# Performance work log

Measured on AMD Instinct MI355X. Metric: run time of the kernel, lower is better.

## Reference

```python
import jax, jax.numpy as jnp
import numpy as np

DIM = 1024
NUM_HEADS = 16
HEAD_DIM = DIM // NUM_HEADS
B, NQ, NKV = 8, 1024, 1024


def setup_inputs() -> dict:
    key = jax.random.key(0)
    ks = jax.random.split(key, 6)
    std = 1.0 / np.sqrt(DIM)
    return {
        "x": jax.random.normal(ks[0], (B, NQ, DIM), dtype=jnp.float32),
        "context": jax.random.normal(ks[1], (B, NKV, DIM), dtype=jnp.float32),
        "Wq": jax.random.normal(ks[2], (DIM, DIM), dtype=jnp.float32) * std,
        "bq": jnp.zeros((DIM,), dtype=jnp.float32),
        "Wk": jax.random.normal(ks[3], (DIM, DIM), dtype=jnp.float32) * std,
        "bk": jnp.zeros((DIM,), dtype=jnp.float32),
        "Wv": jax.random.normal(ks[4], (DIM, DIM), dtype=jnp.float32) * std,
        "bv": jnp.zeros((DIM,), dtype=jnp.float32),
        "Wo": jax.random.normal(ks[5], (DIM, DIM), dtype=jnp.float32) * std,
        "bo": jnp.zeros((DIM,), dtype=jnp.float32),
    }


def _split_heads(t):
    # [B, N, D] -> [B, H, N, Hd]
    b, n, _ = t.shape
    return t.reshape(b, n, NUM_HEADS, HEAD_DIM).transpose(0, 2, 1, 3)


def reference(x, context, Wq, bq, Wk, bk, Wv, bv, Wo, bo):
    scale = HEAD_DIM ** -0.5
    q = _split_heads(x @ Wq + bq)        # [B,H,Nq,Hd]
    k = _split_heads(context @ Wk + bk)  # [B,H,Nk,Hd]
    v = _split_heads(context @ Wv + bv)  # [B,H,Nk,Hd]
    # scaled dot-product attention
    scores = jnp.einsum("bhqd,bhkd->bhqk", q, k) * scale
    attn = jax.nn.softmax(scores, axis=-1)
    out = jnp.einsum("bhqk,bhkd->bhqd", attn, v)  # [B,H,Nq,Hd]
    out = out.transpose(0, 2, 1, 3).reshape(x.shape[0], x.shape[1], DIM)
    return out @ Wo + bo
```

## Files before the change

kernel.cpp:

```cpp
#include <hip/hip_runtime.h>
#include <stdint.h>

using bf16x8 = __attribute__((ext_vector_type(8))) short;
using f32x4  = __attribute__((ext_vector_type(4))) float;
using f32x2  = __attribute__((ext_vector_type(2))) float;
using u16    = unsigned short;
using u16x4  = __attribute__((ext_vector_type(4))) unsigned short;
using u16x8  = __attribute__((ext_vector_type(8))) unsigned short;
using bf16x2v = __attribute__((ext_vector_type(2))) __bf16;

#define LOG2E 1.4426950408889634f

static __device__ __forceinline__ u16 bf16r(float f) {
  union { __bf16 h; u16 u; } v; v.h = (__bf16)f; return v.u;
}
static __device__ __forceinline__ unsigned pk2(float a, float b) {
  union { bf16x2v h; unsigned u; } r;
  r.h = __builtin_convertvector((f32x2){a, b}, bf16x2v);
  return r.u;
}
static __device__ __forceinline__ u16x4 pk4(float a, float b, float c, float d) {
  union { unsigned u[2]; u16x4 v; } r;
  r.u[0] = pk2(a, b); r.u[1] = pk2(c, d);
  return r.v;
}

static __device__ __forceinline__ void async_ld16(u16* lds, const u16* g) {
  __builtin_amdgcn_global_load_lds(
      (const __attribute__((address_space(1))) void*)g,
      (__attribute__((address_space(3))) void*)lds,
      16, 0, 0);
}

static __device__ __forceinline__ f32x4 mfma16(bf16x8 a, bf16x8 b, f32x4 c) {
  return __builtin_amdgcn_mfma_f32_16x16x32_bf16(a, b, c, 0, 0, 0);
}

__global__ void prep_kernel(const float* __restrict__ x, const float* __restrict__ ctx,
                            const float* __restrict__ W0, const float* __restrict__ W1,
                            const float* __restrict__ W2, const float* __restrict__ W3,
                            u16* __restrict__ Xb, u16* __restrict__ Cb,
                            u16* __restrict__ T0, u16* __restrict__ T1,
                            u16* __restrict__ T2, u16* __restrict__ T3) {
  int bid = blockIdx.x;
  int t = threadIdx.x;
  if (bid < 4096) {
    const int n4 = 2097152;
    int i = bid * 256 + t;
    const int stride = 4096 * 256;
#pragma unroll
    for (int it = 0; it < 4; ++it, i += stride) {
      const float4* src = (i < n4) ? ((const float4*)x + i) : ((const float4*)ctx + (i - n4));
      u16x4* dst = (i < n4) ? ((u16x4*)Xb + i) : ((u16x4*)Cb + (i - n4));
      float4 v = *src;
      *dst = pk4(v.x, v.y, v.z, v.w);
    }
    return;
  }
  int b2 = bid - 4096;
  int z = b2 >> 8, rem = b2 & 255;
  const float* W = (z == 0) ? W0 : (z == 1) ? W1 : (z == 2) ? W2 : W3;
  u16* T = (z == 0) ? T0 : (z == 1) ? T1 : (z == 2) ? T2 : T3;
  __shared__ float tile[64][65];
  int k0 = (rem & 15) * 64, n0 = (rem >> 4) * 64;
#pragma unroll
  for (int i = 0; i < 4; ++i) {
    int kl = i * 16 + (t >> 4); int nl = (t & 15) * 4;
    float4 v = *(const float4*)(W + (size_t)(k0 + kl) * 1024 + n0 + nl);
    tile[kl][nl] = v.x; tile[kl][nl + 1] = v.y; tile[kl][nl + 2] = v.z; tile[kl][nl + 3] = v.w;
  }
  __syncthreads();
#pragma unroll
  for (int i = 0; i < 16; ++i) {
    int idx = i * 256 + t; int nl = idx >> 6; int kl = idx & 63;
    T[(size_t)(n0 + nl) * 1024 + k0 + kl] = bf16r(tile[kl][nl]);
  }
}

__global__ __launch_bounds__(256) void proj_gemm_kernel(
    const u16* __restrict__ Xb, const u16* __restrict__ Cb,
    const u16* __restrict__ Wqt, const u16* __restrict__ Wkt, const u16* __restrict__ Wvt,
    const float* __restrict__ bq, const float* __restrict__ bk, const float* __restrict__ bv,
    u16* __restrict__ Qo, u16* __restrict__ Ko, u16* __restrict__ Vo) {
  __shared__ u16 smem[16896];
  u16* sA = smem;
  u16* sB = smem + 8192;
  int z = blockIdx.z;
  const u16* A    = (z == 0) ? Xb : Cb;
  const u16* Bt   = (z == 0) ? Wqt : (z == 1) ? Wkt : Wvt;
  const float* bias = (z == 0) ? bq : (z == 1) ? bk : bv;
  int m0 = blockIdx.x * 128, n0 = blockIdx.y * 128;
  int t = threadIdx.x, w = t >> 6, lane = t & 63, quad = lane >> 4, lc = lane & 15;
  int wm = (w & 1) * 64, wn = (w >> 1) * 64;
  int sx = lc & 7;

  f32x4 acc[4][4];
  f32x4 z4 = {0.f, 0.f, 0.f, 0.f};
#pragma unroll
  for (int i = 0; i < 4; ++i)
#pragma unroll
    for (int j = 0; j < 4; ++j) acc[i][j] = z4;

  int srow = t >> 3;
  int swz  = (t & 7) ^ (srow & 7);
  const u16* Ag = A  + (size_t)(m0 + srow) * 1024 + swz * 8;
  const u16* Bg = Bt + (size_t)(n0 + srow) * 1024 + swz * 8;
  u16* la = sA + t * 8;
  u16* lb = sB + t * 8;

  for (int kt = 0; kt < 16; ++kt) {
    __syncthreads();
#pragma unroll
    for (int i = 0; i < 4; ++i) {
      async_ld16(la + i * 2048, Ag + (size_t)i * 32 * 1024);
      async_ld16(lb + i * 2048, Bg + (size_t)i * 32 * 1024);
    }
    Ag += 64; Bg += 64;
    asm volatile("s_waitcnt vmcnt(0)" ::: "memory");
    __syncthreads();
#pragma unroll
    for (int ks = 0; ks < 2; ++ks) {
      bf16x8 af[4], bfr[4];
#pragma unroll
      for (int i = 0; i < 4; ++i)
        af[i]  = *(const bf16x8*)(sA + (wm + i * 16 + lc) * 64 + (((ks * 4 + quad) ^ sx)) * 8);
#pragma unroll
      for (int i = 0; i < 4; ++i)
        bfr[i] = *(const bf16x8*)(sB + (wn + i * 16 + lc) * 64 + (((ks * 4 + quad) ^ sx)) * 8);
#pragma unroll
      for (int qi = 0; qi < 4; ++qi)
#pragma unroll
        for (int nj = 0; nj < 4; ++nj) acc[qi][nj] = mfma16(af[qi], bfr[nj], acc[qi][nj]);
    }
  }

  if (z < 2) {
    u16* dst = (z == 0) ? Qo : Ko;
    float scl = (z == 0) ? 0.125f * LOG2E : 1.0f;
#pragma unroll
    for (int qi = 0; qi < 4; ++qi)
#pragma unroll
      for (int nj = 0; nj < 4; ++nj) {
        int n = n0 + wn + nj * 16 + lc;
        float bvv = bias[n];
        int hh = n >> 6, d = n & 63;
#pragma unroll
        for (int r = 0; r < 4; ++r) {
          int m = m0 + wm + qi * 16 + quad * 4 + r;
          int bb = m >> 10, pos = m & 1023;
          float v = (acc[qi][nj][r] + bvv) * scl;
          dst[((size_t)(bb * 16 + hh) * 1024 + pos) * 64 + d] = bf16r(v);
        }
      }
  } else {
    __syncthreads();
    u16* Tw = smem + w * (64 * 66);
    int hh = (n0 + wn) >> 6;
    int mb = m0 + wm; int bb = mb >> 10; int pos0 = mb & 1023;
#pragma unroll
    for (int qi = 0; qi < 4; ++qi)
#pragma unroll
      for (int nj = 0; nj < 4; ++nj) {
        int lcc = nj * 16 + lc;
        float bvv = bias[n0 + wn + lcc];
#pragma unroll
        for (int r = 0; r < 4; ++r) {
          int lr = qi * 16 + quad * 4 + r;
          Tw[lr * 66 + lcc] = bf16r(acc[qi][nj][r] + bvv);
        }
      }
#pragma unroll
    for (int i = 0; i < 8; ++i) {
      int dl = i * 8 + (lane >> 3); int kv0 = (lane & 7) * 8;
      u16x8 pk;
#pragma unroll
      for (int j = 0; j < 8; ++j) pk[j] = Tw[(kv0 + j) * 66 + dl];
      *(u16x8*)(Vo + ((size_t)(bb * 16 + hh) * 64 + dl) * 1024 + pos0 + kv0) = pk;
    }
  }
}

__global__ __launch_bounds__(256, 3) void attn_kernel(const u16* __restrict__ Qb,
                                                      const u16* __restrict__ Kb,
                                                      const u16* __restrict__ Vt,
                                                      u16* __restrict__ Ab) {
  __shared__ u16 smem[24576];
  u16* sP = smem + 16384;
  int bid = blockIdx.x;
  int bh = (bid & 7) | ((bid >> 6) << 3);
  int qt = (bid >> 3) & 7;
  int bb = bh >> 4, hh = bh & 15;
  int t = threadIdx.x, w = t >> 6, lane = t & 63, quad = lane >> 4, lc = lane & 15;

  const u16* Qg = Qb + ((size_t)bh * 1024 + qt * 128 + w * 32) * 64;
  bf16x8 qf[2][2];
#pragma unroll
  for (int qi = 0; qi < 2; ++qi)
#pragma unroll
    for (int ks = 0; ks < 2; ++ks)
      qf[qi][ks] = *(const bf16x8*)(Qg + (qi * 16 + lc) * 64 + ks * 32 + quad * 8);

  f32x4 O[4][2];
  f32x4 z4 = {0.f, 0.f, 0.f, 0.f};
#pragma unroll
  for (int dj = 0; dj < 4; ++dj) { O[dj][0] = z4; O[dj][1] = z4; }
  float l_lane[2] = {0.f, 0.f};

  const u16* Kg = Kb + (size_t)bh * 65536;
  const u16* Vg = Vt + (size_t)bh * 65536;
  int r0 = t >> 3, gs = t & 7;

  auto STAGE = [&](int b, int kt) {
    u16* sKb = smem + b * 8192;
    u16* sVb = sKb + 4096;
#pragma unroll
    for (int i = 0; i < 2; ++i) {
      int r = r0 + i * 32;
      async_ld16(sKb + i * 2048 + t * 8, Kg + (size_t)(kt * 64 + r) * 64 + (gs ^ (r & 7)) * 8);
    }
#pragma unroll
    for (int i = 0; i < 2; ++i) {
      int d = r0 + i * 32;
      async_ld16(sVb + i * 2048 + t * 8, Vg + (size_t)d * 1024 + kt * 64 + (gs ^ (d & 7)) * 8);
    }
  };

  STAGE(0, 0);

  for (int kt = 0; kt < 16; ++kt) {
    int cur = kt & 1;
    __builtin_amdgcn_s_barrier();
    if (kt < 15) {
      STAGE(cur ^ 1, kt + 1);
      asm volatile("s_waitcnt vmcnt(8)" ::: "memory");
    } else {
      asm volatile("s_waitcnt vmcnt(0)" ::: "memory");
    }
    __builtin_amdgcn_s_barrier();

    const u16* sK = smem + cur * 8192;
    const u16* sV = sK + 4096;

    f32x4 s[4][2];
#pragma unroll
    for (int kj = 0; kj < 4; ++kj) { s[kj][0] = z4; s[kj][1] = z4; }
    __builtin_amdgcn_s_setprio(1);
#pragma unroll
    for (int kj = 0; kj < 4; ++kj) {
      int kv = kj * 16 + lc;
#pragma unroll
      for (int ks = 0; ks < 2; ++ks) {
        bf16x8 a = *(const bf16x8*)(sK + kv * 64 + ((ks * 4 + quad) ^ (kv & 7)) * 8);
        s[kj][0] = mfma16(a, qf[0][ks], s[kj][0]);
        s[kj][1] = mfma16(a, qf[1][ks], s[kj][1]);
      }
    }
    __builtin_amdgcn_s_setprio(0);

#pragma unroll
    for (int qi = 0; qi < 2; ++qi) {
      int q = w * 32 + qi * 16 + lc;
#pragma unroll
      for (int kj = 0; kj < 4; ++kj) {
        float p0 = exp2f(s[kj][qi][0]);
        float p1 = exp2f(s[kj][qi][1]);
        float p2 = exp2f(s[kj][qi][2]);
        float p3 = exp2f(s[kj][qi][3]);
        l_lane[qi] += (p0 + p1) + (p2 + p3);
        int g = kj * 2 + (quad >> 1);
        *(u16x4*)(sP + q * 64 + ((g ^ (q & 7)) * 8) + (quad & 1) * 4) = pk4(p0, p1, p2, p3);
      }
    }

    __builtin_amdgcn_s_setprio(1);
#pragma unroll
    for (int ks = 0; ks < 2; ++ks) {
      bf16x8 pb[2];
#pragma unroll
      for (int qi = 0; qi < 2; ++qi) {
        int q = w * 32 + qi * 16 + lc;
        pb[qi] = *(const bf16x8*)(sP + q * 64 + (((ks * 4 + quad) ^ (q & 7))) * 8);
      }
#pragma unroll
      for (int dj = 0; dj < 4; ++dj) {
        int d = dj * 16 + lc;
        bf16x8 va = *(const bf16x8*)(sV + d * 64 + (((ks * 4 + quad) ^ (d & 7))) * 8);
        O[dj][0] = mfma16(va, pb[0], O[dj][0]);
        O[dj][1] = mfma16(va, pb[1], O[dj][1]);
      }
    }
    __builtin_amdgcn_s_setprio(0);
  }

  float inv[2];
#pragma unroll
  for (int qi = 0; qi < 2; ++qi) {
    float l = l_lane[qi];
    l += __shfl_xor(l, 16);
    l += __shfl_xor(l, 32);
    inv[qi] = 1.f / l;
  }

  __syncthreads();
  u16* myP = smem + w * 2304;
#pragma unroll
  for (int qi = 0; qi < 2; ++qi)
#pragma unroll
    for (int dj = 0; dj < 4; ++dj)
      *(u16x4*)(myP + (qi * 16 + lc) * 72 + dj * 16 + quad * 4) =
          pk4(O[dj][qi][0] * inv[qi], O[dj][qi][1] * inv[qi],
              O[dj][qi][2] * inv[qi], O[dj][qi][3] * inv[qi]);
#pragma unroll
  for (int i = 0; i < 4; ++i) {
    int idx = i * 64 + lane; int ql = idx >> 3; int dg = idx & 7;
    u16x8 pk = *(const u16x8*)(myP + ql * 72 + dg * 8);
    *(u16x8*)(Ab + ((size_t)bb * 1024 + qt * 128 + w * 32 + ql) * 1024 + hh * 64 + dg * 8) = pk;
  }
}

__global__ __launch_bounds__(256) void out_gemm_kernel(const u16* __restrict__ A,
                                                       const u16* __restrict__ Bt,
                                                       const float* __restrict__ bo,
                                                       float* __restrict__ out) {
  __shared__ u16 smem[16384];
  u16* sA = smem;
  u16* sB = smem + 8192;
  int m0 = blockIdx.x * 128, n0 = blockIdx.y * 128;
  int t = threadIdx.x, w = t >> 6, lane = t & 63, quad = lane >> 4, lc = lane & 15;
  int wm = (w & 1) * 64, wn = (w >> 1) * 64;
  int sx = lc & 7;
  f32x4 acc[4][4];
  f32x4 z4 = {0.f, 0.f, 0.f, 0.f};
#pragma unroll
  for (int i = 0; i < 4; ++i)
#pragma unroll
    for (int j = 0; j < 4; ++j) acc[i][j] = z4;
  int srow = t >> 3;
  int swz  = (t & 7) ^ (srow & 7);
  const u16* Ag = A  + (size_t)(m0 + srow) * 1024 + swz * 8;
  const u16* Bg = Bt + (size_t)(n0 + srow) * 1024 + swz * 8;
  u16* la = sA + t * 8;
  u16* lb = sB + t * 8;
  for (int kt = 0; kt < 16; ++kt) {
    __syncthreads();
#pragma unroll
    for (int i = 0; i < 4; ++i) {
      async_ld16(la + i * 2048, Ag + (size_t)i * 32 * 1024);
      async_ld16(lb + i * 2048, Bg + (size_t)i * 32 * 1024);
    }
    Ag += 64; Bg += 64;
    asm volatile("s_waitcnt vmcnt(0)" ::: "memory");
    __syncthreads();
#pragma unroll
    for (int ks = 0; ks < 2; ++ks) {
      bf16x8 af[4], bfr[4];
#pragma unroll
      for (int i = 0; i < 4; ++i)
        af[i]  = *(const bf16x8*)(sA + (wm + i * 16 + lc) * 64 + (((ks * 4 + quad) ^ sx)) * 8);
#pragma unroll
      for (int i = 0; i < 4; ++i)
        bfr[i] = *(const bf16x8*)(sB + (wn + i * 16 + lc) * 64 + (((ks * 4 + quad) ^ sx)) * 8);
#pragma unroll
      for (int qi = 0; qi < 4; ++qi)
#pragma unroll
        for (int nj = 0; nj < 4; ++nj) acc[qi][nj] = mfma16(af[qi], bfr[nj], acc[qi][nj]);
    }
  }
#pragma unroll
  for (int qi = 0; qi < 4; ++qi)
#pragma unroll
    for (int nj = 0; nj < 4; ++nj) {
      int n = n0 + wn + nj * 16 + lc;
      float bvv = bo[n];
#pragma unroll
      for (int r = 0; r < 4; ++r) {
        int m = m0 + wm + qi * 16 + quad * 4 + r;
        out[(size_t)m * 1024 + n] = acc[qi][nj][r] + bvv;
      }
    }
}

extern "C" void kernel_launch(void* const* d_in, const int* in_sizes, int n_in,
                              void* d_out, int out_size, void* d_ws, size_t ws_size,
                              hipStream_t stream) {
  const float* x   = (const float*)d_in[0];
  const float* ctx = (const float*)d_in[1];
  const float* Wq  = (const float*)d_in[2];
  const float* bq  = (const float*)d_in[3];
  const float* Wk  = (const float*)d_in[4];
  const float* bk  = (const float*)d_in[5];
  const float* Wv  = (const float*)d_in[6];
  const float* bv  = (const float*)d_in[7];
  const float* Wo  = (const float*)d_in[8];
  const float* bo  = (const float*)d_in[9];
  float* out = (float*)d_out;

  const size_t NE = (size_t)8192 * 1024;
  char* p = (char*)d_ws;
  u16* Xb  = (u16*)p;             p += NE * 2;
  u16* Cb  = (u16*)p;             p += NE * 2;
  u16* Wqt = (u16*)p;             p += (size_t)1024 * 1024 * 2;
  u16* Wkt = (u16*)p;             p += (size_t)1024 * 1024 * 2;
  u16* Wvt = (u16*)p;             p += (size_t)1024 * 1024 * 2;
  u16* Wot = (u16*)p;             p += (size_t)1024 * 1024 * 2;
  u16* Qb  = (u16*)p;             p += NE * 2;
  u16* Kb  = (u16*)p;             p += NE * 2;
  u16* Vtb = (u16*)p;             p += NE * 2;
  u16* Ab  = Xb;

  prep_kernel<<<5120, 256, 0, stream>>>(x, ctx, Wq, Wk, Wv, Wo,
                                        Xb, Cb, Wqt, Wkt, Wvt, Wot);
  proj_gemm_kernel<<<dim3(64, 8, 3), 256, 0, stream>>>(Xb, Cb, Wqt, Wkt, Wvt,
                                                       bq, bk, bv, Qb, Kb, Vtb);
  attn_kernel<<<1024, 256, 0, stream>>>(Qb, Kb, Vtb, Ab);
  out_gemm_kernel<<<dim3(64, 8), 256, 0, stream>>>(Ab, Wot, bo, out);
}
```

Before: 269.2 us.

## Double-buffer LDS tiles in projection and output GEMMs with async prefetch

```diff
diff --git a/kernel.cpp b/kernel.cpp
--- a/kernel.cpp
+++ b/kernel.cpp
@@ -77,14 +77,14 @@
   }
 }
 
-__global__ __launch_bounds__(256) void proj_gemm_kernel(
+__global__ __launch_bounds__(256, 2) void proj_gemm_kernel(
     const u16* __restrict__ Xb, const u16* __restrict__ Cb,
     const u16* __restrict__ Wqt, const u16* __restrict__ Wkt, const u16* __restrict__ Wvt,
     const float* __restrict__ bq, const float* __restrict__ bk, const float* __restrict__ bv,
     u16* __restrict__ Qo, u16* __restrict__ Ko, u16* __restrict__ Vo) {
-  __shared__ u16 smem[16896];
+  __shared__ u16 smem[32768];
   u16* sA = smem;
-  u16* sB = smem + 8192;
+  u16* sB = smem + 16384;
   int z = blockIdx.z;
   const u16* A    = (z == 0) ? Xb : Cb;
   const u16* Bt   = (z == 0) ? Wqt : (z == 1) ? Wkt : Wvt;
@@ -101,37 +101,52 @@
 #pragma unroll
     for (int j = 0; j < 4; ++j) acc[i][j] = z4;
 
-  int srow = t >> 3;
-  int swz  = (t & 7) ^ (srow & 7);
-  const u16* Ag = A  + (size_t)(m0 + srow) * 1024 + swz * 8;
-  const u16* Bg = Bt + (size_t)(n0 + srow) * 1024 + swz * 8;
-  u16* la = sA + t * 8;
-  u16* lb = sB + t * 8;
+  const u16* Abase = A  + (size_t)m0 * 1024;
+  const u16* Bbase = Bt + (size_t)n0 * 1024;
+
+  auto STAGE = [&](int s, int kt) {
+#pragma unroll
+    for (int i = 0; i < 4; ++i) {
+      int c = i * 256 + t; int row = c >> 3; int cc = c & 7;
+      async_ld16(sA + s * 8192 + c * 8,
+                 Abase + (size_t)row * 1024 + kt * 64 + ((cc ^ (row & 7)) * 8));
+    }
+#pragma unroll
+    for (int i = 0; i < 4; ++i) {
+      int c = i * 256 + t; int row = c >> 3; int cc = c & 7;
+      async_ld16(sB + s * 8192 + c * 8,
+                 Bbase + (size_t)row * 1024 + kt * 64 + ((cc ^ (row & 7)) * 8));
+    }
+  };
+
+  STAGE(0, 0);
+  STAGE(1, 1);
 
   for (int kt = 0; kt < 16; ++kt) {
-    __syncthreads();
-#pragma unroll
-    for (int i = 0; i < 4; ++i) {
-      async_ld16(la + i * 2048, Ag + (size_t)i * 32 * 1024);
-      async_ld16(lb + i * 2048, Bg + (size_t)i * 32 * 1024);
-    }
-    Ag += 64; Bg += 64;
-    asm volatile("s_waitcnt vmcnt(0)" ::: "memory");
-    __syncthreads();
+    int s = kt & 1;
+    if (kt < 15) asm volatile("s_waitcnt vmcnt(8)" ::: "memory");
+    else         asm volatile("s_waitcnt vmcnt(0)" ::: "memory");
+    __builtin_amdgcn_s_barrier();
+    const u16* pA = sA + s * 8192;
+    const u16* pB = sB + s * 8192;
 #pragma unroll
     for (int ks = 0; ks < 2; ++ks) {
       bf16x8 af[4], bfr[4];
 #pragma unroll
       for (int i = 0; i < 4; ++i)
-        af[i]  = *(const bf16x8*)(sA + (wm + i * 16 + lc) * 64 + (((ks * 4 + quad) ^ sx)) * 8);
+        af[i]  = *(const bf16x8*)(pA + (wm + i * 16 + lc) * 64 + (((ks * 4 + quad) ^ sx)) * 8);
 #pragma unroll
       for (int i = 0; i < 4; ++i)
-        bfr[i] = *(const bf16x8*)(sB + (wn + i * 16 + lc) * 64 + (((ks * 4 + quad) ^ sx)) * 8);
+        bfr[i] = *(const bf16x8*)(pB + (wn + i * 16 + lc) * 64 + (((ks * 4 + quad) ^ sx)) * 8);
+      __builtin_amdgcn_s_setprio(1);
 #pragma unroll
       for (int qi = 0; qi < 4; ++qi)
 #pragma unroll
         for (int nj = 0; nj < 4; ++nj) acc[qi][nj] = mfma16(af[qi], bfr[nj], acc[qi][nj]);
-    }
+      __builtin_amdgcn_s_setprio(0);
+    }
+    __builtin_amdgcn_s_barrier();
+    if (kt < 14) STAGE(s, kt + 2);
   }
 
   if (z < 2) {
@@ -318,13 +333,13 @@
   }
 }
 
-__global__ __launch_bounds__(256) void out_gemm_kernel(const u16* __restrict__ A,
-                                                       const u16* __restrict__ Bt,
-                                                       const float* __restrict__ bo,
-                                                       float* __restrict__ out) {
-  __shared__ u16 smem[16384];
+__global__ __launch_bounds__(256, 2) void out_gemm_kernel(const u16* __restrict__ A,
+                                                          const u16* __restrict__ Bt,
+                                                          const float* __restrict__ bo,
+                                                          float* __restrict__ out) {
+  __shared__ u16 smem[32768];
   u16* sA = smem;
-  u16* sB = smem + 8192;
+  u16* sB = smem + 16384;
   int m0 = blockIdx.x * 128, n0 = blockIdx.y * 128;
   int t = threadIdx.x, w = t >> 6, lane = t & 63, quad = lane >> 4, lc = lane & 15;
   int wm = (w & 1) * 64, wn = (w >> 1) * 64;
@@ -335,37 +350,55 @@
   for (int i = 0; i < 4; ++i)
 #pragma unroll
     for (int j = 0; j < 4; ++j) acc[i][j] = z4;
-  int srow = t >> 3;
-  int swz  = (t & 7) ^ (srow & 7);
-  const u16* Ag = A  + (size_t)(m0 + srow) * 1024 + swz * 8;
-  const u16* Bg = Bt + (size_t)(n0 + srow) * 1024 + swz * 8;
-  u16* la = sA + t * 8;
-  u16* lb = sB + t * 8;
+
+  const u16* Abase = A  + (size_t)m0 * 1024;
+  const u16* Bbase = Bt + (size_t)n0 * 1024;
+
+  auto STAGE = [&](int s, int kt) {
+#pragma unroll
+    for (int i = 0; i < 4; ++i) {
+      int c = i * 256 + t; int row = c >> 3; int cc = c & 7;
+      async_ld16(sA + s * 8192 + c * 8,
+                 Abase + (size_t)row * 1024 + kt * 64 + ((cc ^ (row & 7)) * 8));
+    }
+#pragma unroll
+    for (int i = 0; i < 4; ++i) {
+      int c = i * 256 + t; int row = c >> 3; int cc = c & 7;
+      async_ld16(sB + s * 8192 + c * 8,
+                 Bbase + (size_t)row * 1024 + kt * 64 + ((cc ^ (row & 7)) * 8));
+    }
+  };
+
+  STAGE(0, 0);
+  STAGE(1, 1);
+
   for (int kt = 0; kt < 16; ++kt) {
-    __syncthreads();
-#pragma unroll
-    for (int i = 0; i < 4; ++i) {
-      async_ld16(la + i * 2048, Ag + (size_t)i * 32 * 1024);
-      async_ld16(lb + i * 2048, Bg + (size_t)i * 32 * 1024);
-    }
-    Ag += 64; Bg += 64;
-    asm volatile("s_waitcnt vmcnt(0)" ::: "memory");
-    __syncthreads();
+    int s = kt & 1;
+    if (kt < 15) asm volatile("s_waitcnt vmcnt(8)" ::: "memory");
+    else         asm volatile("s_waitcnt vmcnt(0)" ::: "memory");
+    __builtin_amdgcn_s_barrier();
+    const u16* pA = sA + s * 8192;
+    const u16* pB = sB + s * 8192;
 #pragma unroll
     for (int ks = 0; ks < 2; ++ks) {
       bf16x8 af[4], bfr[4];
 #pragma unroll
       for (int i = 0; i < 4; ++i)
-        af[i]  = *(const bf16x8*)(sA + (wm + i * 16 + lc) * 64 + (((ks * 4 + quad) ^ sx)) * 8);
+        af[i]  = *(const bf16x8*)(pA + (wm + i * 16 + lc) * 64 + (((ks * 4 + quad) ^ sx)) * 8);
 #pragma unroll
       for (int i = 0; i < 4; ++i)
-        bfr[i] = *(const bf16x8*)(sB + (wn + i * 16 + lc) * 64 + (((ks * 4 + quad) ^ sx)) * 8);
+        bfr[i] = *(const bf16x8*)(pB + (wn + i * 16 + lc) * 64 + (((ks * 4 + quad) ^ sx)) * 8);
+      __builtin_amdgcn_s_setprio(1);
 #pragma unroll
       for (int qi = 0; qi < 4; ++qi)
 #pragma unroll
         for (int nj = 0; nj < 4; ++nj) acc[qi][nj] = mfma16(af[qi], bfr[nj], acc[qi][nj]);
-    }
-  }
+      __builtin_amdgcn_s_setprio(0);
+    }
+    __builtin_amdgcn_s_barrier();
+    if (kt < 14) STAGE(s, kt + 2);
+  }
+
 #pragma unroll
   for (int qi = 0; qi < 4; ++qi)
 #pragma unroll
```

After: 262.1 us. 1.03x faster.
